# Kernel tuning notes

Hardware: AMD Instinct MI355X
Metric: run time of the kernel (lower is better)

The kernel has to match this reference:

```python
import jax, jax.numpy as jnp
import numpy as np

B, IN_DIM = 64, 256
R, L = 2, 2                    # rank, num_mlp_layers
D1A, D2A = 1024, 512           # w1 shape
D1B, D2B = 512, 1024           # w2 shape
H, O = 3072, 1536              # hyper hidden = int(sum(shape)*2.0), out = sum(shape)


def setup_inputs() -> dict:
    key = jax.random.key(0)
    ks = iter(jax.random.split(key, 20))

    def rn(shape, s=0.02):
        return jax.random.normal(next(ks), shape, dtype=jnp.float32) * s

    inp = {
        "u_0": jax.random.normal(next(ks), (B, IN_DIM), dtype=jnp.float32),
        "w1": rn((D1A, D2A)),
        "w2": rn((D1B, D2B)),
    }
    for n in ("w1", "w2"):
        inp[f"win_{n}"] = rn((R, H, IN_DIM))
        inp[f"bin_{n}"] = rn((R, H))
        inp[f"hw_{n}"] = rn((R, L, H, H))
        inp[f"hb_{n}"] = rn((R, L, H))
        inp[f"wout_{n}"] = rn((R, O, H))
        inp[f"bout_{n}"] = rn((R, O))
    return inp


def _gelu(x):
    # torch F.gelu default = exact erf-based gelu
    return jax.nn.gelu(x, approximate=False)


def _mlp_apply(x, win, b_in, hw, hb, wout, b_out):
    # MLP_net_variable with use_act=False, use_dropout=False
    h = _gelu(x @ win.T + b_in)              # [B, H]
    for l in range(hw.shape[0]):             # small fixed num_layers
        h = _gelu(h @ hw[l].T + hb[l])
    return h @ wout.T + b_out                # [B, O], no final activation


def _synth(vec_u, base, win, b_in, hw, hb, wout, b_out):
    d1, d2 = base.shape
    # vmap the per-rank MLPs over the stacked rank axis -> flat [R, B, d1+d2]
    flat = jax.vmap(lambda W, b, HW, HB, WO, BO: _mlp_apply(vec_u, W, b, HW, HB, WO, BO))(
        win, b_in, hw, hb, wout, b_out)
    v1, v2 = flat[..., :d1], flat[..., d1:]  # split along feature dim (torch .split)
    # sum over rank of per-batch outer products, added once to the base param
    return base[None] + jnp.einsum('rbi,rbj->bij', v1, v2)


def reference(u_0, w1, w2,
              win_w1, bin_w1, hw_w1, hb_w1, wout_w1, bout_w1,
              win_w2, bin_w2, hw_w2, hb_w2, wout_w2, bout_w2):
    vec_u = u_0.reshape(u_0.shape[0], -1)    # [B, in_dim]
    new_w1 = _synth(vec_u, w1, win_w1, bin_w1, hw_w1, hb_w1, wout_w1, bout_w1)
    new_w2 = _synth(vec_u, w2, win_w2, bin_w2, hw_w2, hb_w2, wout_w2, bout_w2)
    return (new_w1, new_w2)
```

## Files before the change

kernel.cpp:

```cpp
#include <hip/hip_runtime.h>
#include <hip/hip_bf16.h>

typedef float f32x4 __attribute__((ext_vector_type(4)));
typedef short s16x8 __attribute__((ext_vector_type(8)));
typedef short s16x4 __attribute__((ext_vector_type(4)));

#define THREADS 256

__device__ __forceinline__ unsigned short f2bf(float f) {
  union { float f; unsigned int u; } v;
  v.f = f;
  unsigned int u = v.u;
  u += 0x7fffu + ((u >> 16) & 1u);
  return (unsigned short)(u >> 16);
}

struct GemmArgs {
  const float* W[4];
  const float* Bi[4];
};

template<bool GELU, bool OUTBF16>
__global__ __launch_bounds__(THREADS, 3) void mlp_gemm(
    const unsigned short* __restrict__ X, unsigned long long xstride,
    GemmArgs args,
    void* __restrict__ Y, unsigned long long ystride,
    int N, int K)
{
  constexpr int NT = 16;
  constexpr int KC = 256;
  __shared__ __align__(16) unsigned short Wb[2][NT * KC];

  const int e    = blockIdx.y;
  const int n0   = blockIdx.x * NT;
  const int t    = threadIdx.x;
  const int lane = t & 63;
  const int wid  = t >> 6;

  const float* __restrict__ Wg = args.W[e];
  const unsigned short* __restrict__ Xg = X + (size_t)e * xstride;

  const int srow = wid;
  const int skq  = lane;

  auto load_st = [&](f32x4 (&s)[4], int k0) {
#pragma unroll
    for (int rd = 0; rd < 4; ++rd) {
      const int row = rd * 4 + srow;
      s[rd] = *(const f32x4*)(Wg + (size_t)(n0 + row) * K + k0 + skq * 4);
    }
  };

  auto write_st = [&](int bi, const f32x4 (&s)[4]) {
    unsigned short* lds = Wb[bi];
#pragma unroll
    for (int rd = 0; rd < 4; ++rd) {
      const int row = rd * 4 + srow;
      const int off = row * KC + ((((skq >> 1) ^ (row & 7)) << 3) | ((skq & 1) << 2));
      s16x4 p;
      p[0] = (short)f2bf(s[rd][0]);
      p[1] = (short)f2bf(s[rd][1]);
      p[2] = (short)f2bf(s[rd][2]);
      p[3] = (short)f2bf(s[rd][3]);
      *(s16x4*)(lds + off) = p;
    }
  };

  f32x4 acc = {0.f, 0.f, 0.f, 0.f};

  const int arow = wid * 16 + (lane & 15);
  const unsigned short* __restrict__ xrow = Xg + (size_t)arow * K + ((lane >> 4) << 3);
  const int brow = lane & 15;
  const int bch  = lane >> 4;

  auto compute = [&](int bi, int kg) {
    const unsigned short* lds = Wb[bi];
    s16x8 af[8];
#pragma unroll
    for (int i = 0; i < 8; ++i)
      af[i] = *(const s16x8*)(xrow + kg + i * 32);
#pragma unroll
    for (int i = 0; i < 8; ++i) {
      const int ch = ((i << 2) + bch) ^ (brow & 7);
      s16x8 b = *(const s16x8*)(lds + brow * KC + ch * 8);
      acc = __builtin_amdgcn_mfma_f32_16x16x32_bf16(af[i], b, acc, 0, 0, 0);
    }
  };

  const int NCH = K / KC;

  f32x4 sA[4], sB[4];
  load_st(sA, 0);
  if (NCH > 1) load_st(sB, KC);
  write_st(0, sA);
  __syncthreads();

  for (int c = 0; c < NCH; ++c) {
    const bool even = !(c & 1);
    if (c + 2 < NCH) {
      if (even) load_st(sA, (c + 2) * KC);
      else      load_st(sB, (c + 2) * KC);
    }
    compute(c & 1, c * KC);
    if (c + 1 < NCH) {
      if (even) write_st(1, sB);
      else      write_st(0, sA);
    }
    __syncthreads();
  }

  const float* __restrict__ Bi = args.Bi[e];
  const int col   = lane & 15;
  const int nn    = n0 + col;
  const int rbase = wid * 16 + ((lane >> 4) << 2);
  const float bv  = Bi[nn];
#pragma unroll
  for (int r = 0; r < 4; ++r) {
    float yv = acc[r] + bv;
    if (GELU) yv = 0.5f * yv * (1.0f + erff(yv * 0.70710678118654752f));
    const size_t oidx = (size_t)e * ystride + (size_t)(rbase + r) * N + nn;
    if (OUTBF16) ((unsigned short*)Y)[oidx] = f2bf(yv);
    else         ((float*)Y)[oidx] = yv;
  }
}

__global__ __launch_bounds__(THREADS) void cvt_u_kernel(
    const float* __restrict__ u, unsigned short* __restrict__ ub)
{
  const int i = blockIdx.x * THREADS + threadIdx.x;
  ub[i] = f2bf(u[i]);
}

template<int D1, int D2>
__global__ __launch_bounds__(THREADS) void synth_kernel(
    const float* __restrict__ Wbase, const float* __restrict__ V,
    float* __restrict__ Out)
{
  constexpr int QPR = D2 / 4;
  constexpr int RP  = THREADS / QPR;
  constexpr size_t S = (size_t)64 * 1536;
  const int b    = blockIdx.y;
  const int i0   = blockIdx.x * 32;
  const int isub = threadIdx.x / QPR;
  const int jq   = threadIdx.x % QPR;
  const float* __restrict__ vb = V + (size_t)b * 1536;
  const f32x4 v2a = *(const f32x4*)(vb + D1 + jq * 4);
  const f32x4 v2b = *(const f32x4*)(vb + S + D1 + jq * 4);
#pragma unroll
  for (int ii = isub; ii < 32; ii += RP) {
    const int i = i0 + ii;
    const float a0 = vb[i];
    const float a1 = vb[S + i];
    const f32x4 w = *(const f32x4*)(Wbase + (size_t)i * D2 + jq * 4);
    f32x4 o = w + a0 * v2a + a1 * v2b;
    *(f32x4*)(Out + ((size_t)b * D1 + i) * D2 + jq * 4) = o;
  }
}

extern "C" void kernel_launch(void* const* d_in, const int* in_sizes, int n_in,
                              void* d_out, int out_size, void* d_ws, size_t ws_size,
                              hipStream_t stream) {
  const int Hh = 3072, IND = 256, OD = 1536;

  const float* u0  = (const float*)d_in[0];
  const float* w1  = (const float*)d_in[1];
  const float* w2  = (const float*)d_in[2];
  const float* win[2] = {(const float*)d_in[3], (const float*)d_in[9]};
  const float* bin[2] = {(const float*)d_in[4], (const float*)d_in[10]};
  const float* hw [2] = {(const float*)d_in[5], (const float*)d_in[11]};
  const float* hb [2] = {(const float*)d_in[6], (const float*)d_in[12]};
  const float* wou[2] = {(const float*)d_in[7], (const float*)d_in[13]};
  const float* bou[2] = {(const float*)d_in[8], (const float*)d_in[14]};

  char* ws = (char*)d_ws;
  unsigned short* ub = (unsigned short*)ws;
  unsigned short* hA = (unsigned short*)(ws + (64 << 10));
  unsigned short* hB = (unsigned short*)(ws + (64 << 10) + (2 << 20));
  float*          vv = (float*)(ws + (64 << 10) + (4 << 20));

  cvt_u_kernel<<<64, THREADS, 0, stream>>>(u0, ub);

  GemmArgs ga;
  for (int e = 0; e < 4; ++e) {
    const int n = e >> 1, r = e & 1;
    ga.W[e]  = win[n] + (size_t)r * Hh * IND;
    ga.Bi[e] = bin[n] + (size_t)r * Hh;
  }
  mlp_gemm<true, true><<<dim3(Hh / 16, 4), THREADS, 0, stream>>>(
      ub, 0ull, ga, hA, (unsigned long long)64 * Hh, Hh, IND);

  for (int l = 0; l < 2; ++l) {
    for (int e = 0; e < 4; ++e) {
      const int n = e >> 1, r = e & 1;
      ga.W[e]  = hw[n] + (size_t)(r * 2 + l) * Hh * Hh;
      ga.Bi[e] = hb[n] + (size_t)(r * 2 + l) * Hh;
    }
    const unsigned short* xin = (l == 0) ? hA : hB;
    unsigned short*      yout = (l == 0) ? hB : hA;
    mlp_gemm<true, true><<<dim3(Hh / 16, 4), THREADS, 0, stream>>>(
        xin, (unsigned long long)64 * Hh, ga, yout, (unsigned long long)64 * Hh, Hh, Hh);
  }

  for (int e = 0; e < 4; ++e) {
    const int n = e >> 1, r = e & 1;
    ga.W[e]  = wou[n] + (size_t)r * OD * Hh;
    ga.Bi[e] = bou[n] + (size_t)r * OD;
  }
  mlp_gemm<false, false><<<dim3(OD / 16, 4), THREADS, 0, stream>>>(
      hA, (unsigned long long)64 * Hh, ga, vv, (unsigned long long)64 * OD, OD, Hh);

  float* out = (float*)d_out;
  synth_kernel<1024, 512><<<dim3(1024 / 32, 64), THREADS, 0, stream>>>(w1, vv, out);
  synth_kernel<512, 1024><<<dim3(512 / 32, 64), THREADS, 0, stream>>>(
      w2, vv + (size_t)2 * 64 * 1536, out + (size_t)64 * 1024 * 512);
}
```

Baseline: 653.5 us.

## Replace LDS-staged GEMM with single-wave register-streamed MFMA and fuse synth launches

Each GEMM block becomes one 64-thread wave that streams its 16 weight rows straight from global memory into registers, converts them to bf16, and reuses each B fragment across four 16-row M tiles via four accumulators. This removes the LDS staging, the double buffering and the block barriers. The two synth kernels are merged into one launch that selects the shape on blockIdx.z. The risk is less latency hiding for the weight stream, since loads are no longer staged ahead of use, and less per-block parallelism, in exchange for fewer syncs and fewer launches.

```diff
diff --git a/kernel.cpp b/kernel.cpp
--- a/kernel.cpp
+++ b/kernel.cpp
@@ -3,9 +3,6 @@
 
 typedef float f32x4 __attribute__((ext_vector_type(4)));
 typedef short s16x8 __attribute__((ext_vector_type(8)));
-typedef short s16x4 __attribute__((ext_vector_type(4)));
-
-#define THREADS 256
 
 __device__ __forceinline__ unsigned short f2bf(float f) {
   union { float f; unsigned int u; } v;
@@ -21,126 +18,82 @@
 };
 
 template<bool GELU, bool OUTBF16>
-__global__ __launch_bounds__(THREADS, 3) void mlp_gemm(
+__global__ __launch_bounds__(64) void mlp_gemm(
     const unsigned short* __restrict__ X, unsigned long long xstride,
     GemmArgs args,
     void* __restrict__ Y, unsigned long long ystride,
     int N, int K)
 {
-  constexpr int NT = 16;
-  constexpr int KC = 256;
-  __shared__ __align__(16) unsigned short Wb[2][NT * KC];
-
   const int e    = blockIdx.y;
-  const int n0   = blockIdx.x * NT;
-  const int t    = threadIdx.x;
-  const int lane = t & 63;
-  const int wid  = t >> 6;
+  const int n0   = blockIdx.x * 16;
+  const int lane = threadIdx.x & 63;
 
   const float* __restrict__ Wg = args.W[e];
   const unsigned short* __restrict__ Xg = X + (size_t)e * xstride;
 
-  const int srow = wid;
-  const int skq  = lane;
+  const int frow = lane & 15;
+  const int bk8  = (lane >> 4) << 3;
 
-  auto load_st = [&](f32x4 (&s)[4], int k0) {
+  const float*          __restrict__ wrow = Wg + (size_t)(n0 + frow) * K + bk8;
+  const unsigned short* __restrict__ xrow = Xg + (size_t)frow * K + bk8;
+  const size_t mstride = (size_t)16 * K;
+
+  f32x4 acc[4];
 #pragma unroll
-    for (int rd = 0; rd < 4; ++rd) {
-      const int row = rd * 4 + srow;
-      s[rd] = *(const f32x4*)(Wg + (size_t)(n0 + row) * K + k0 + skq * 4);
+  for (int m = 0; m < 4; ++m) acc[m] = {0.f, 0.f, 0.f, 0.f};
+
+#pragma unroll 4
+  for (int k = 0; k < K; k += 32) {
+    const f32x4 wlo = *(const f32x4*)(wrow + k);
+    const f32x4 whi = *(const f32x4*)(wrow + k + 4);
+    s16x8 b;
+    b[0] = (short)f2bf(wlo[0]); b[1] = (short)f2bf(wlo[1]);
+    b[2] = (short)f2bf(wlo[2]); b[3] = (short)f2bf(wlo[3]);
+    b[4] = (short)f2bf(whi[0]); b[5] = (short)f2bf(whi[1]);
+    b[6] = (short)f2bf(whi[2]); b[7] = (short)f2bf(whi[3]);
+#pragma unroll
+    for (int m = 0; m < 4; ++m) {
+      const s16x8 a = *(const s16x8*)(xrow + (size_t)m * mstride + k);
+      acc[m] = __builtin_amdgcn_mfma_f32_16x16x32_bf16(a, b, acc[m], 0, 0, 0);
     }
-  };
-
-  auto write_st = [&](int bi, const f32x4 (&s)[4]) {
-    unsigned short* lds = Wb[bi];
-#pragma unroll
-    for (int rd = 0; rd < 4; ++rd) {
-      const int row = rd * 4 + srow;
-      const int off = row * KC + ((((skq >> 1) ^ (row & 7)) << 3) | ((skq & 1) << 2));
-      s16x4 p;
-      p[0] = (short)f2bf(s[rd][0]);
-      p[1] = (short)f2bf(s[rd][1]);
-      p[2] = (short)f2bf(s[rd][2]);
-      p[3] = (short)f2bf(s[rd][3]);
-      *(s16x4*)(lds + off) = p;
-    }
-  };
-
-  f32x4 acc = {0.f, 0.f, 0.f, 0.f};
-
-  const int arow = wid * 16 + (lane & 15);
-  const unsigned short* __restrict__ xrow = Xg + (size_t)arow * K + ((lane >> 4) << 3);
-  const int brow = lane & 15;
-  const int bch  = lane >> 4;
-
-  auto compute = [&](int bi, int kg) {
-    const unsigned short* lds = Wb[bi];
-    s16x8 af[8];
-#pragma unroll
-    for (int i = 0; i < 8; ++i)
-      af[i] = *(const s16x8*)(xrow + kg + i * 32);
-#pragma unroll
-    for (int i = 0; i < 8; ++i) {
-      const int ch = ((i << 2) + bch) ^ (brow & 7);
-      s16x8 b = *(const s16x8*)(lds + brow * KC + ch * 8);
-      acc = __builtin_amdgcn_mfma_f32_16x16x32_bf16(af[i], b, acc, 0, 0, 0);
-    }
-  };
-
-  const int NCH = K / KC;
-
-  f32x4 sA[4], sB[4];
-  load_st(sA, 0);
-  if (NCH > 1) load_st(sB, KC);
-  write_st(0, sA);
-  __syncthreads();
-
-  for (int c = 0; c < NCH; ++c) {
-    const bool even = !(c & 1);
-    if (c + 2 < NCH) {
-      if (even) load_st(sA, (c + 2) * KC);
-      else      load_st(sB, (c + 2) * KC);
-    }
-    compute(c & 1, c * KC);
-    if (c + 1 < NCH) {
-      if (even) write_st(1, sB);
-      else      write_st(0, sA);
-    }
-    __syncthreads();
   }
 
   const float* __restrict__ Bi = args.Bi[e];
-  const int col   = lane & 15;
-  const int nn    = n0 + col;
-  const int rbase = wid * 16 + ((lane >> 4) << 2);
-  const float bv  = Bi[nn];
+  const int col = lane & 15;
+  const int nn  = n0 + col;
+  const float bv = Bi[nn];
+  const int rsub = (lane >> 4) << 2;
 #pragma unroll
-  for (int r = 0; r < 4; ++r) {
-    float yv = acc[r] + bv;
-    if (GELU) yv = 0.5f * yv * (1.0f + erff(yv * 0.70710678118654752f));
-    const size_t oidx = (size_t)e * ystride + (size_t)(rbase + r) * N + nn;
-    if (OUTBF16) ((unsigned short*)Y)[oidx] = f2bf(yv);
-    else         ((float*)Y)[oidx] = yv;
+  for (int m = 0; m < 4; ++m) {
+#pragma unroll
+    for (int r = 0; r < 4; ++r) {
+      float yv = acc[m][r] + bv;
+      if (GELU) yv = 0.5f * yv * (1.0f + erff(yv * 0.70710678118654752f));
+      const size_t oidx = (size_t)e * ystride + (size_t)(m * 16 + rsub + r) * N + nn;
+      if (OUTBF16) ((unsigned short*)Y)[oidx] = f2bf(yv);
+      else         ((float*)Y)[oidx] = yv;
+    }
   }
 }
 
-__global__ __launch_bounds__(THREADS) void cvt_u_kernel(
+__global__ __launch_bounds__(256) void cvt_u_kernel(
     const float* __restrict__ u, unsigned short* __restrict__ ub)
 {
-  const int i = blockIdx.x * THREADS + threadIdx.x;
+  const int i = blockIdx.x * 256 + threadIdx.x;
   ub[i] = f2bf(u[i]);
 }
 
 template<int D1, int D2>
-__global__ __launch_bounds__(THREADS) void synth_kernel(
+__device__ __forceinline__ void synth_body(
     const float* __restrict__ Wbase, const float* __restrict__ V,
     float* __restrict__ Out)
 {
   constexpr int QPR = D2 / 4;
-  constexpr int RP  = THREADS / QPR;
+  constexpr int RP  = 256 / QPR;
   constexpr size_t S = (size_t)64 * 1536;
+  const int i0 = blockIdx.x * 32;
+  if (i0 >= D1) return;
   const int b    = blockIdx.y;
-  const int i0   = blockIdx.x * 32;
   const int isub = threadIdx.x / QPR;
   const int jq   = threadIdx.x % QPR;
   const float* __restrict__ vb = V + (size_t)b * 1536;
@@ -154,6 +107,18 @@
     const f32x4 w = *(const f32x4*)(Wbase + (size_t)i * D2 + jq * 4);
     f32x4 o = w + a0 * v2a + a1 * v2b;
     *(f32x4*)(Out + ((size_t)b * D1 + i) * D2 + jq * 4) = o;
+  }
+}
+
+__global__ __launch_bounds__(256) void synth_fused(
+    const float* __restrict__ w1, const float* __restrict__ w2,
+    const float* __restrict__ V, float* __restrict__ Out)
+{
+  if (blockIdx.z == 0) {
+    synth_body<1024, 512>(w1, V, Out);
+  } else {
+    synth_body<512, 1024>(w2, V + (size_t)2 * 64 * 1536,
+                          Out + (size_t)64 * 1024 * 512);
   }
 }
 
@@ -178,7 +143,7 @@
   unsigned short* hB = (unsigned short*)(ws + (64 << 10) + (2 << 20));
   float*          vv = (float*)(ws + (64 << 10) + (4 << 20));
 
-  cvt_u_kernel<<<64, THREADS, 0, stream>>>(u0, ub);
+  cvt_u_kernel<<<64, 256, 0, stream>>>(u0, ub);
 
   GemmArgs ga;
   for (int e = 0; e < 4; ++e) {
@@ -186,7 +151,7 @@
     ga.W[e]  = win[n] + (size_t)r * Hh * IND;
     ga.Bi[e] = bin[n] + (size_t)r * Hh;
   }
-  mlp_gemm<true, true><<<dim3(Hh / 16, 4), THREADS, 0, stream>>>(
+  mlp_gemm<true, true><<<dim3(Hh / 16, 4), 64, 0, stream>>>(
       ub, 0ull, ga, hA, (unsigned long long)64 * Hh, Hh, IND);
 
   for (int l = 0; l < 2; ++l) {
@@ -197,7 +162,7 @@
     }
     const unsigned short* xin = (l == 0) ? hA : hB;
     unsigned short*      yout = (l == 0) ? hB : hA;
-    mlp_gemm<true, true><<<dim3(Hh / 16, 4), THREADS, 0, stream>>>(
+    mlp_gemm<true, true><<<dim3(Hh / 16, 4), 64, 0, stream>>>(
         xin, (unsigned long long)64 * Hh, ga, yout, (unsigned long long)64 * Hh, Hh, Hh);
   }
 
@@ -206,11 +171,9 @@
     ga.W[e]  = wou[n] + (size_t)r * OD * Hh;
     ga.Bi[e] = bou[n] + (size_t)r * OD;
   }
-  mlp_gemm<false, false><<<dim3(OD / 16, 4), THREADS, 0, stream>>>(
+  mlp_gemm<false, false><<<dim3(OD / 16, 4), 64, 0, stream>>>(
       hA, (unsigned long long)64 * Hh, ga, vv, (unsigned long long)64 * OD, OD, Hh);
 
   float* out = (float*)d_out;
-  synth_kernel<1024, 512><<<dim3(1024 / 32, 64), THREADS, 0, stream>>>(w1, vv, out);
-  synth_kernel<512, 1024><<<dim3(512 / 32, 64), THREADS, 0, stream>>>(
-      w2, vv + (size_t)2 * 64 * 1536, out + (size_t)64 * 1024 * 512);
+  synth_fused<<<dim3(32, 64, 2), 256, 0, stream>>>(w1, w2, vv, out);
 }
```

Result: slower. 909.9 us (+39.2%).
